# Kernel tuning notes

Hardware: AMD Instinct MI355X
Metric: run time of the kernel (lower is better)

## Reference

```python
import jax, jax.numpy as jnp
import numpy as np

STRIDE, PAD, DIL = 1, 1, 1  # from init_kwargs
RELU = True


def setup_inputs() -> dict:
    key = jax.random.key(0)
    k1, k2, k3 = jax.random.split(key, 3)
    B, Cin, Cout, H, W, K = 32, 128, 256, 56, 56, 3
    # uint8 quantized codes stored as float32 (module does .float() before conv)
    x = jnp.round(jax.random.uniform(k1, (B, Cin, H, W), dtype=jnp.float32) * 255.0)
    weight = jnp.round(jax.random.uniform(k2, (Cout, Cin, K, K), dtype=jnp.float32) * 255.0)
    # int32 quantized bias (scale = s_x * s_w, zero_point = 0)
    bias = jnp.round(jax.random.normal(k3, (Cout,), dtype=jnp.float32) * 1000.0)
    return {
        "x": x,
        "weight": weight,
        "bias": bias,
        "M": jnp.float32(0.0021),      # s_x * s_w / s_y
        "x_zero": jnp.float32(128.0),
        "w_zero": jnp.float32(127.0),
        "y_zero": jnp.float32(0.0),
    }


def reference(x, weight, bias, M, x_zero, w_zero, y_zero):
    # x: [B, Cin, H, W] uint8 codes as float; weight: [Cout, Cin, kh, kw]
    xz = x - x_zero                    # zero-point sub (padding adds literal 0s, as in torch: pad AFTER sub)
    w = weight - w_zero
    y = jax.lax.conv_general_dilated(
        xz, w,
        window_strides=(STRIDE, STRIDE),
        padding=((PAD, PAD), (PAD, PAD)),
        rhs_dilation=(DIL, DIL),
        dimension_numbers=("NCHW", "OIHW", "NCHW"),
    )
    y = (y + bias[None, :, None, None]) * M + y_zero  # requantize
    if RELU:
        y = jnp.maximum(y, y_zero)     # clamp below at output zero-point
    return jnp.round(y)
```

## Files before the change

kernel.cpp:

```cpp
#include <hip/hip_runtime.h>
#include <hip/hip_bf16.h>


typedef __attribute__((ext_vector_type(4))) int   i32x4;
typedef __attribute__((ext_vector_type(4))) float f32x4;

#define WTI8_BYTES (18 * 16384)
#define XPI8_BYTES (32 * 58 * 8192)

__device__ __forceinline__ void gload_lds16(const void* g, void* l) {
    __builtin_amdgcn_global_load_lds(
        (const __attribute__((address_space(1))) void*)g,
        (__attribute__((address_space(3))) void*)l, 16, 0, 0);
}

__global__ void wprep_kernel(const float* __restrict__ w, char* __restrict__ wt) {
    int cidx = blockIdx.x * 256 + threadIdx.x;
    int blob = cidx >> 10;
    int e    = cidx & 1023;
    int byte0 = e * 16;
    int rr  = byte0 >> 8;
    int off = byte0 & 255;
    int src = off ^ ((rr & 7) << 4);
    int q   = src >> 6;
    int kl0 = src & 63;
    int r = blob >> 1, ch = blob & 1;
    int n = q * 64 + rr;
    union { char c[16]; i32x4 v; } u;
#pragma unroll
    for (int j = 0; j < 16; ++j) {
        int cin = ch * 64 + kl0 + j;
        u.c[j] = (char)((int)w[(size_t)n * 1152 + cin * 9 + r] - 128);
    }
    *(i32x4*)(wt + (size_t)blob * 16384 + byte0) = u.v;
}

__global__ void xprep_kernel(const float* __restrict__ x, const float* __restrict__ xzp,
                             char* __restrict__ xpi8, int* __restrict__ colsum) {
    int bhh = blockIdx.x;
    int b = bhh / 58, hh = bhh % 58;
    int tid = threadIdx.x;
    char* blob = xpi8 + (size_t)bhh * 8192;
    int w  = tid & 63;
    int cq = tid >> 6;
    __shared__ int ps[4][64];
    if (hh == 0 || hh == 57) {
        i32x4 z = {0, 0, 0, 0};
        *(i32x4*)(blob + tid * 32)      = z;
        *(i32x4*)(blob + tid * 32 + 16) = z;
        if (cq == 0) colsum[bhh * 64 + w] = 0;
        return;
    }
    const int ZX = (int)rintf(*xzp);
    bool valid = (w >= 1 && w <= 56);
    const float* xb = x + (size_t)b * 128 * 3136 + (size_t)(hh - 1) * 56 +
                      (valid ? (w - 1) : 0);
    int csum = 0;
#pragma unroll
    for (int u = 0; u < 2; ++u) {
        union { char c[16]; i32x4 v; } uu;
#pragma unroll
        for (int j = 0; j < 16; ++j) {
            int c = cq * 32 + u * 16 + j;
            int val = valid ? ((int)xb[(size_t)c * 3136] - ZX) : 0;
            uu.c[j] = (char)val;
            csum += val;
        }
        *(i32x4*)(blob + w * 128 + ((cq * 32 + u * 16) ^ ((w & 7) << 4))) = uu.v;
    }
    ps[cq][w] = csum;
    __syncthreads();
    if (cq == 0)
        colsum[bhh * 64 + w] = ps[0][w] + ps[1][w] + ps[2][w] + ps[3][w];
}

__global__ __launch_bounds__(512, 2)
void conv_kernel(const char* __restrict__ wt,
                 const char* __restrict__ xpi8,
                 const int* __restrict__ colsum,
                 const float* __restrict__ bias,
                 const float* __restrict__ Mp,
                 const float* __restrict__ wzp,
                 const float* __restrict__ yzp,
                 float* __restrict__ out) {
    __shared__ __align__(1024) char smem[81920];
    __shared__ int s2row[4][64];
    char* As = smem;
    char* Bs = smem + 49152;

    const int tid = threadIdx.x;
    const int lane = tid & 63;
    const int wid = tid >> 6;
    const int wm = wid >> 2;
    const int wn = wid & 3;
    const int l15 = lane & 15, lg = lane >> 4;
    const int bx = blockIdx.x;
    const int b = bx / 14;
    const int h0 = (bx % 14) * 4;

    const char* agbase = xpi8 + (size_t)(b * 58 + h0) * 8192;
#pragma unroll
    for (int i = 0; i < 6; ++i)
        gload_lds16(agbase + i * 8192 + tid * 16, As + i * 8192 + tid * 16);
#pragma unroll
    for (int i = 0; i < 2; ++i)
        gload_lds16(wt + i * 8192 + tid * 16, Bs + i * 8192 + tid * 16);
    if (tid < 256) {
        int row = tid >> 6, m = tid & 63;
        int s = 0;
        if (m < 56) {
#pragma unroll
            for (int kh = 0; kh < 3; ++kh)
#pragma unroll
                for (int kw = 0; kw < 3; ++kw)
                    s += colsum[(b * 58 + h0 + row + kh) * 64 + m + kw];
        }
        s2row[row][m] = s;
    }

    i32x4 acc[4][8];
#pragma unroll
    for (int i = 0; i < 4; ++i)
#pragma unroll
        for (int j = 0; j < 8; ++j)
            acc[i][j] = (i32x4){0, 0, 0, 0};

    __syncthreads();

#pragma unroll
    for (int s = 0; s < 18; ++s) {
        if (s < 17) {
            const char* src = wt + (size_t)(s + 1) * 16384;
            char* dst = Bs + ((s + 1) & 1) * 16384;
#pragma unroll
            for (int i = 0; i < 2; ++i)
                gload_lds16(src + i * 8192 + tid * 16, dst + i * 8192 + tid * 16);
        }
        const int kh = (s >> 1) / 3, kw = (s >> 1) % 3, ch = s & 1;
        i32x4 bfr[4];
#pragma unroll
        for (int fn = 0; fn < 4; ++fn) {
            int rr = fn * 16 + l15;
            int bb = (s & 1) * 16384 + rr * 256 +
                     ((wn * 64 + lg * 16) ^ ((rr & 7) << 4));
            bfr[fn] = *(const i32x4*)(Bs + bb);
        }
        i32x4 afr[8];
#pragma unroll
        for (int fm = 0; fm < 8; ++fm) {
            int rowoff = fm >> 2;
            int wv = (fm & 3) * 16 + l15 + kw;
            int wc = wv > 63 ? 63 : wv;
            int ab = (wm * 2 + rowoff + kh) * 8192 + wc * 128 +
                     ((ch * 64 + lg * 16) ^ ((wc & 7) << 4));
            afr[fm] = *(const i32x4*)(As + ab);
        }
#pragma unroll
        for (int fn = 0; fn < 4; ++fn)
#pragma unroll
            for (int fm = 0; fm < 8; ++fm)
                acc[fn][fm] = __builtin_amdgcn_mfma_i32_16x16x64_i8(
                    bfr[fn], afr[fm], acc[fn][fm], 0, 0, 0);
        __syncthreads();
    }

    const float Mv  = *Mp;
    const float yzv = *yzp;
    const float CWf = 128.0f - *wzp;
#pragma unroll
    for (int fn = 0; fn < 4; ++fn) {
#pragma unroll
        for (int reg = 0; reg < 4; ++reg) {
            const int cout = wn * 64 + fn * 16 + lg * 4 + reg;
            const float bv = bias[cout];
#pragma unroll
            for (int fm = 0; fm < 8; ++fm) {
                const int row = wm * 2 + (fm >> 2);
                const int m = (fm & 3) * 16 + l15;
                if (m < 56) {
                    const size_t rowb =
                        ((size_t)(b * 256 + cout) * 56 + h0 + row) * 56;
                    float af = (float)acc[fn][fm][reg] +
                               CWf * (float)s2row[row][m];
                    float v = (af + bv) * Mv + yzv;
                    v = fmaxf(v, yzv);
                    out[rowb + m] = rintf(v);
                }
            }
        }
    }
}

extern "C" void kernel_launch(void* const* d_in, const int* in_sizes, int n_in,
                              void* d_out, int out_size, void* d_ws, size_t ws_size,
                              hipStream_t stream) {
    const float* x    = (const float*)d_in[0];
    const float* w    = (const float*)d_in[1];
    const float* bias = (const float*)d_in[2];
    const float* Mp   = (const float*)d_in[3];
    const float* xzp  = (const float*)d_in[4];
    const float* wzp  = (const float*)d_in[5];
    const float* yzp  = (const float*)d_in[6];
    float* out = (float*)d_out;

    char* wt     = (char*)d_ws;
    char* xpi8   = wt + WTI8_BYTES;
    int*  colsum = (int*)(xpi8 + XPI8_BYTES);

    wprep_kernel<<<72, 256, 0, stream>>>(w, wt);
    xprep_kernel<<<32 * 58, 256, 0, stream>>>(x, xzp, xpi8, colsum);
    conv_kernel<<<32 * 14, 512, 0, stream>>>(wt, xpi8, colsum, bias, Mp, wzp, yzp, out);
}
```

Baseline: 79.78 us.

## Give each wave private triple-buffered weight tiles and drop per-stage block barriers

```diff
diff --git a/kernel.cpp b/kernel.cpp
--- a/kernel.cpp
+++ b/kernel.cpp
@@ -16,23 +16,22 @@
 
 __global__ void wprep_kernel(const float* __restrict__ w, char* __restrict__ wt) {
     int cidx = blockIdx.x * 256 + threadIdx.x;
-    int blob = cidx >> 10;
-    int e    = cidx & 1023;
-    int byte0 = e * 16;
-    int rr  = byte0 >> 8;
-    int off = byte0 & 255;
-    int src = off ^ ((rr & 7) << 4);
-    int q   = src >> 6;
-    int kl0 = src & 63;
-    int r = blob >> 1, ch = blob & 1;
-    int n = q * 64 + rr;
+    int byte0 = cidx * 16;
+    int s    = byte0 >> 14;
+    int wn   = (byte0 >> 12) & 3;
+    int e4   = byte0 & 4095;
+    int nn   = e4 >> 6;
+    int koff = e4 & 63;
+    int kl   = koff ^ ((nn & 3) << 4);
+    int n = wn * 64 + nn;
+    int r = s >> 1, ch = s & 1;
     union { char c[16]; i32x4 v; } u;
 #pragma unroll
     for (int j = 0; j < 16; ++j) {
-        int cin = ch * 64 + kl0 + j;
+        int cin = ch * 64 + kl + j;
         u.c[j] = (char)((int)w[(size_t)n * 1152 + cin * 9 + r] - 128);
     }
-    *(i32x4*)(wt + (size_t)blob * 16384 + byte0) = u.v;
+    *(i32x4*)(wt + byte0) = u.v;
 }
 
 __global__ void xprep_kernel(const float* __restrict__ x, const float* __restrict__ xzp,
@@ -74,7 +73,7 @@
         colsum[bhh * 64 + w] = ps[0][w] + ps[1][w] + ps[2][w] + ps[3][w];
 }
 
-__global__ __launch_bounds__(512, 2)
+__global__ __launch_bounds__(512, 1)
 void conv_kernel(const char* __restrict__ wt,
                  const char* __restrict__ xpi8,
                  const int* __restrict__ colsum,
@@ -83,10 +82,9 @@
                  const float* __restrict__ wzp,
                  const float* __restrict__ yzp,
                  float* __restrict__ out) {
-    __shared__ __align__(1024) char smem[81920];
+    __shared__ __align__(1024) char As[49152];
+    __shared__ __align__(1024) char Bp[98304];
     __shared__ int s2row[4][64];
-    char* As = smem;
-    char* Bs = smem + 49152;
 
     const int tid = threadIdx.x;
     const int lane = tid & 63;
@@ -98,13 +96,19 @@
     const int b = bx / 14;
     const int h0 = (bx % 14) * 4;
 
+    char* bpriv = Bp + wid * 12288;
+    const char* bwsrc = wt + wn * 4096 + lane * 16;
+
     const char* agbase = xpi8 + (size_t)(b * 58 + h0) * 8192;
 #pragma unroll
     for (int i = 0; i < 6; ++i)
         gload_lds16(agbase + i * 8192 + tid * 16, As + i * 8192 + tid * 16);
 #pragma unroll
-    for (int i = 0; i < 2; ++i)
-        gload_lds16(wt + i * 8192 + tid * 16, Bs + i * 8192 + tid * 16);
+    for (int st = 0; st < 2; ++st)
+#pragma unroll
+        for (int i = 0; i < 4; ++i)
+            gload_lds16(bwsrc + (size_t)st * 16384 + i * 1024,
+                        bpriv + st * 4096 + i * 1024 + lane * 16);
     if (tid < 256) {
         int row = tid >> 6, m = tid & 63;
         int s = 0;
@@ -129,21 +133,25 @@
 
 #pragma unroll
     for (int s = 0; s < 18; ++s) {
-        if (s < 17) {
-            const char* src = wt + (size_t)(s + 1) * 16384;
-            char* dst = Bs + ((s + 1) & 1) * 16384;
-#pragma unroll
-            for (int i = 0; i < 2; ++i)
-                gload_lds16(src + i * 8192 + tid * 16, dst + i * 8192 + tid * 16);
-        }
+        if (s < 16) {
+#pragma unroll
+            for (int i = 0; i < 4; ++i)
+                gload_lds16(bwsrc + (size_t)(s + 2) * 16384 + i * 1024,
+                            bpriv + ((s + 2) % 3) * 4096 + i * 1024 + lane * 16);
+        }
+        if (s < 16)      asm volatile("s_waitcnt vmcnt(8)" ::: "memory");
+        else if (s == 16) asm volatile("s_waitcnt vmcnt(4)" ::: "memory");
+        else              asm volatile("s_waitcnt vmcnt(0)" ::: "memory");
+        __builtin_amdgcn_sched_barrier(0);
+
         const int kh = (s >> 1) / 3, kw = (s >> 1) % 3, ch = s & 1;
+        const char* bslot = bpriv + (s % 3) * 4096;
         i32x4 bfr[4];
 #pragma unroll
         for (int fn = 0; fn < 4; ++fn) {
-            int rr = fn * 16 + l15;
-            int bb = (s & 1) * 16384 + rr * 256 +
-                     ((wn * 64 + lg * 16) ^ ((rr & 7) << 4));
-            bfr[fn] = *(const i32x4*)(Bs + bb);
+            int nn = fn * 16 + l15;
+            bfr[fn] = *(const i32x4*)(bslot + nn * 64 +
+                                      ((lg * 16) ^ ((l15 & 3) << 4)));
         }
         i32x4 afr[8];
 #pragma unroll
@@ -161,7 +169,6 @@
             for (int fm = 0; fm < 8; ++fm)
                 acc[fn][fm] = __builtin_amdgcn_mfma_i32_16x16x64_i8(
                     bfr[fn], afr[fm], acc[fn][fm], 0, 0, 0);
-        __syncthreads();
     }
 
     const float Mv  = *Mp;
```

Result: faster. 76.15 us (-4.6%).
